# Optimization experiments

Hardware: AMD Instinct MI355X
Metric: run time of the kernel (lower is better)

The kernel has to match this reference:

```python
import jax, jax.numpy as jnp
import numpy as np
from jax import lax

B, N, S, K = 8, 8192, 2048, 32
CPTS = 64
RADIUS = 0.25
MLP = [64, 64, 128]
EPS = 1e-5


def fps(xyz, npoint):
    # furthest point sampling, starts at index 0 (pointnet2 convention)
    Bn, Nn, _ = xyz.shape

    def step(carry, _):
        mind, last = carry  # mind [B,N], last [B]
        lastp = jnp.take_along_axis(xyz, last[:, None, None], axis=1)  # [B,1,3]
        d = jnp.sum((xyz - lastp) ** 2, axis=-1)  # [B,N]
        mind = jnp.minimum(mind, d)
        nxt = jnp.argmax(mind, axis=-1).astype(jnp.int32)
        return (mind, nxt), last

    init = (jnp.full((Bn, Nn), 1e10, xyz.dtype), jnp.zeros((Bn,), jnp.int32))
    _, idxs = lax.scan(step, init, None, length=npoint)  # [npoint,B]
    return jnp.transpose(idxs)  # [B,npoint]


def ball_query(radius, nsample, xyz, new_xyz):
    # returns first `nsample` indices within radius of each centroid,
    # padding with the first valid index (pointnet2 semantics)
    Nn = xyz.shape[1]
    qq = jnp.sum(new_xyz ** 2, -1)[:, :, None]          # [B,S,1]
    pp = jnp.sum(xyz ** 2, -1)[:, None, :]              # [B,1,N]
    d2 = qq + pp - 2.0 * jnp.einsum('bsc,bnc->bsn', new_xyz, xyz)  # [B,S,N]
    key = jnp.where(d2 <= radius * radius,
                    jnp.arange(Nn, dtype=jnp.int32), jnp.int32(Nn))
    srt = jnp.sort(key, axis=-1)[..., :nsample]          # first valid indices
    return jnp.where(srt < Nn, srt, srt[..., :1])        # pad with first


def _gather(feats, idx):
    # feats [B,N,C], idx [B,S,K] -> [B,S,K,C]
    return jax.vmap(lambda p, i: p[i])(feats, idx)


def setup_inputs() -> dict:
    key = jax.random.key(0)
    ks = jax.random.split(key, 2 + len(MLP))
    xyz = jax.random.normal(ks[0], (B, N, 3), jnp.float32)
    points = jax.random.normal(ks[1], (B, N, CPTS), jnp.float32)
    out = {"xyz": xyz, "points": points}
    cin = 3 + CPTS
    for i, m in enumerate(MLP):
        out[f"w{i}"] = jax.random.normal(ks[2 + i], (m, cin), jnp.float32) * 0.05
        out[f"b{i}"] = jnp.zeros((m,), jnp.float32)
        out[f"g{i}"] = jnp.ones((m,), jnp.float32)
        out[f"be{i}"] = jnp.zeros((m,), jnp.float32)
        cin = m
    return out


def reference(xyz, points, w0, b0, g0, be0, w1, b1, g1, be1, w2, b2, g2, be2):
    fps_idx = fps(xyz, S)                                    # [B,S]
    new_xyz = jnp.take_along_axis(xyz, fps_idx[..., None], axis=1)  # [B,S,3]
    idx = ball_query(RADIUS, K, xyz, new_xyz)                # [B,S,K]

    grouped_xyz = _gather(xyz, idx) - new_xyz[:, :, None, :]  # [B,S,K,3]
    grouped_pts = _gather(points, idx)                        # [B,S,K,CPTS]
    feat = jnp.concatenate([grouped_xyz, grouped_pts], -1)    # [B,S,K,C]

    for (w, b, g, be) in ((w0, b0, g0, be0), (w1, b1, g1, be1), (w2, b2, g2, be2)):
        x = jnp.einsum('bskc,oc->bsko', feat, w) + b           # 1x1 conv
        mean = jnp.mean(x, axis=(0, 1, 2))                     # BN train-mode
        var = jnp.var(x, axis=(0, 1, 2))
        feat = jax.nn.relu((x - mean) * jax.lax.rsqrt(var + EPS) * g + be)

    pooled = jnp.max(feat, axis=2)                             # [B,S,Cout]
    return new_xyz, pooled
```

## Files before the change

kernel.cpp:

```cpp
#include <hip/hip_runtime.h>

#define NPTS 8192
#define NB 8
#define NS 2048
#define NK 32
#define C0 67
#define NTOT (NB*NS*NK)
#define NCONS 248

typedef __attribute__((ext_vector_type(2))) float f32x2;

template <int CTRL, int ROWM>
__device__ __forceinline__ float dpp_fmax_step(float x) {
  int yi = __builtin_amdgcn_update_dpp(__float_as_int(x), __float_as_int(x),
                                       CTRL, ROWM, 0xf, false);
  return fmaxf(x, __int_as_float(yi));
}
template <int CTRL, int ROWM>
__device__ __forceinline__ unsigned dpp_umin_step(unsigned x) {
  unsigned y = (unsigned)__builtin_amdgcn_update_dpp((int)x, (int)x,
                                                     CTRL, ROWM, 0xf, false);
  return (y < x) ? y : x;
}
__device__ __forceinline__ float wave_max_f32(float v) {
  v = dpp_fmax_step<0x111, 0xf>(v);
  v = dpp_fmax_step<0x112, 0xf>(v);
  v = dpp_fmax_step<0x114, 0xf>(v);
  v = dpp_fmax_step<0x118, 0xf>(v);
  v = dpp_fmax_step<0x142, 0xa>(v);
  v = dpp_fmax_step<0x143, 0xc>(v);
  return v;
}
__device__ __forceinline__ unsigned wave_min_u32(unsigned v) {
  v = dpp_umin_step<0x111, 0xf>(v);
  v = dpp_umin_step<0x112, 0xf>(v);
  v = dpp_umin_step<0x114, 0xf>(v);
  v = dpp_umin_step<0x118, 0xf>(v);
  v = dpp_umin_step<0x142, 0xa>(v);
  v = dpp_umin_step<0x143, 0xc>(v);
  return v;
}

union SMemA {
  struct {
    float sx[NPTS], sy[NPTS], sz[NPTS];
    float snx[NS], sny[NS], snz[NS];
    uint2 slotVN[2][4];
  } fps;
  struct {
    float w0t[C0*64];
    float feat[C0*32];
    int   bq[4][32];
    int   bqc[4];
    int   s_idx[32];
    float s_c[3];
  } con;
};

__global__ __launch_bounds__(256, 1) void k_stage1A(
    const float* __restrict__ xyz, const float* __restrict__ pts,
    const float* __restrict__ w0, const float* __restrict__ g0,
    const float* __restrict__ be0,
    float* __restrict__ newxyz, float* __restrict__ pp,
    float* __restrict__ x0, float* __restrict__ part,
    float* __restrict__ statsF, unsigned* __restrict__ sync) {
  __shared__ __align__(16) SMemA sm;
  __shared__ int s_last;
  const int tid = threadIdx.x;
  unsigned* prog = sync;
  unsigned* ctr0 = sync + 8;

  if (blockIdx.x < NB) {
    const int b = blockIdx.x;
    const int wv = tid >> 6, lane = tid & 63;
    const float* Xb = xyz + (size_t)b * NPTS * 3;
    f32x2 px2[16], py2[16], pz2[16], mind2[16];
#pragma unroll
    for (int i = 0; i < 16; i++) {
      int n0 = ((2*i) << 8) | tid;
      int n1 = ((2*i+1) << 8) | tid;
      float ax = Xb[n0*3+0], ay = Xb[n0*3+1], az = Xb[n0*3+2];
      float bx2 = Xb[n1*3+0], by2 = Xb[n1*3+1], bz2 = Xb[n1*3+2];
      px2[i].x = ax;  px2[i].y = bx2;
      py2[i].x = ay;  py2[i].y = by2;
      pz2[i].x = az;  pz2[i].y = bz2;
      sm.fps.sx[n0]=ax;  sm.fps.sy[n0]=ay;  sm.fps.sz[n0]=az;
      sm.fps.sx[n1]=bx2; sm.fps.sy[n1]=by2; sm.fps.sz[n1]=bz2;
      pp[b*NPTS + n0] = __fadd_rn(__fadd_rn(__fmul_rn(ax,ax), __fmul_rn(ay,ay)), __fmul_rn(az,az));
      pp[b*NPTS + n1] = __fadd_rn(__fadd_rn(__fmul_rn(bx2,bx2), __fmul_rn(by2,by2)), __fmul_rn(bz2,bz2));
      mind2[i].x = 1e10f; mind2[i].y = 1e10f;
    }
    __syncthreads();
    float lx = sm.fps.sx[0], ly = sm.fps.sy[0], lz = sm.fps.sz[0];
    if (tid == 0) { sm.fps.snx[0]=lx; sm.fps.sny[0]=ly; sm.fps.snz[0]=lz; }
    for (int s = 1; s < NS; s++) {
#pragma clang fp contract(off)
      f32x2 lxx = {lx, lx}, lyy = {ly, ly}, lzz = {lz, lz};
      f32x2 m16[16];
#pragma unroll
      for (int i = 0; i < 16; i++) {
        f32x2 dx = px2[i] - lxx;
        f32x2 dy = py2[i] - lyy;
        f32x2 dz = pz2[i] - lzz;
        f32x2 d  = (dx*dx + dy*dy) + dz*dz;
        f32x2 m;
        m.x = fminf(mind2[i].x, d.x);
        m.y = fminf(mind2[i].y, d.y);
        mind2[i] = m;
        m16[i] = m;
      }
#pragma unroll
      for (int st = 8; st >= 1; st >>= 1)
#pragma unroll
        for (int i = 0; i < st; i++) {
          m16[i].x = fmaxf(m16[i].x, m16[i+st].x);
          m16[i].y = fmaxf(m16[i].y, m16[i+st].y);
        }
      float v = fmaxf(m16[0].x, m16[0].y);
      float vr = wave_max_f32(v);
      float wmax = __int_as_float(__builtin_amdgcn_readlane(__float_as_int(vr), 63));
      unsigned kt[16];
#pragma unroll
      for (int i = 0; i < 16; i++) {
        unsigned c = (mind2[i].y == v) ? (unsigned)(2*i+1) : 63u;
        kt[i] = (mind2[i].x == v) ? (unsigned)(2*i) : c;
      }
#pragma unroll
      for (int st = 8; st >= 1; st >>= 1)
#pragma unroll
        for (int i = 0; i < st; i++)
          kt[i] = (kt[i] < kt[i+st]) ? kt[i] : kt[i+st];
      unsigned ncand = (v == wmax) ? ((kt[0] << 8) | (unsigned)tid) : 0xffffffffu;
      unsigned nr = wave_min_u32(ncand);
      int buf = s & 1;
      if (lane == 63) sm.fps.slotVN[buf][wv] = make_uint2(__float_as_uint(vr), nr);
      __syncthreads();
      uint4 s01 = *(const uint4*)&sm.fps.slotVN[buf][0];
      uint4 s23 = *(const uint4*)&sm.fps.slotVN[buf][2];
      unsigned bx = s01.x, by = s01.y;
      if (s01.z > bx || (s01.z == bx && s01.w < by)) { bx = s01.z; by = s01.w; }
      if (s23.x > bx || (s23.x == bx && s23.y < by)) { bx = s23.x; by = s23.y; }
      if (s23.z > bx || (s23.z == bx && s23.w < by)) { bx = s23.z; by = s23.w; }
      int n = (int)by;
      lx = sm.fps.sx[n]; ly = sm.fps.sy[n]; lz = sm.fps.sz[n];
      if (tid == 0) { sm.fps.snx[s]=lx; sm.fps.sny[s]=ly; sm.fps.snz[s]=lz; }
      if ((s & 63) == 63) {
        __syncthreads();
        int cs = s - 63;
        if (tid < 192) {
          int e = cs + tid / 3, comp = tid - (tid / 3) * 3;
          float vvv = (comp == 0) ? sm.fps.snx[e] : ((comp == 1) ? sm.fps.sny[e] : sm.fps.snz[e]);
          newxyz[((size_t)b*NS + cs)*3 + tid] = vvv;
        }
        __syncthreads();
        if (tid == 0) {
          __threadfence();
          __hip_atomic_store(&prog[b], (unsigned)(s + 1), __ATOMIC_RELEASE, __HIP_MEMORY_SCOPE_AGENT);
        }
      }
    }
  } else {
    const int cb = blockIdx.x - NB;
    const int wv = tid >> 6, lane = tid & 63;
    float* w0t = sm.con.w0t;
    float* feat = sm.con.feat;
    for (int t = tid; t < C0*64; t += 256) { int j = t >> 6, c = t & 63; w0t[t] = w0[c*C0 + j]; }
    int rt = tid & 7, ct = tid >> 3;
    float s0[2] = {0,0}, q0[2] = {0,0};
    for (int it = 0; it <= 66; it++) {
      int e = cb + NCONS * it;
      if (e >= NB*NS) break;
      int s = e >> 3, b = e & 7;
      size_t row = (size_t)b * NS + s;
      if (tid == 0) {
        while ((int)__hip_atomic_load(&prog[b], __ATOMIC_ACQUIRE, __HIP_MEMORY_SCOPE_AGENT) <= s)
          __builtin_amdgcn_s_sleep(32);
        __threadfence();
      }
      __syncthreads();
      const float* c3 = newxyz + row * 3;
      float cx = c3[0], cy = c3[1], cz = c3[2];
      float qq = __fadd_rn(__fadd_rn(__fmul_rn(cx,cx), __fmul_rn(cy,cy)), __fmul_rn(cz,cz));
      const float* Xb = xyz + (size_t)b * NPTS * 3;
      const float* Pb = pp + b * NPTS;
      int cnt = 0;
      int base = wv << 11;
      for (int j0 = base; j0 < base + 2048; j0 += 64) {
        int n = j0 + lane;
        float x = Xb[n*3+0], y = Xb[n*3+1], z = Xb[n*3+2];
        float dot = __fadd_rn(__fadd_rn(__fmul_rn(cx,x), __fmul_rn(cy,y)), __fmul_rn(cz,z));
        float d2 = __fsub_rn(__fadd_rn(qq, Pb[n]), __fmul_rn(2.0f, dot));
        bool in = (d2 <= 0.0625f);
        unsigned long long bal = __ballot(in);
        if (in) {
          int pos = cnt + (int)__popcll(bal & ((1ull << lane) - 1ull));
          if (pos < NK) sm.con.bq[wv][pos] = n;
        }
        cnt += (int)__popcll(bal);
        if (cnt >= NK) break;
      }
      if (lane == 0) sm.con.bqc[wv] = (cnt < NK) ? cnt : NK;
      __syncthreads();
      if (tid < NK) {
        int l0 = sm.con.bqc[0], l1 = sm.con.bqc[1], l2 = sm.con.bqc[2], l3 = sm.con.bqc[3];
        int t1 = l0 + l1, t2 = t1 + l2, t3 = t2 + l3;
        int j = tid, v;
        if (j < l0)      v = sm.con.bq[0][j];
        else if (j < t1) v = sm.con.bq[1][j - l0];
        else if (j < t2) v = sm.con.bq[2][j - t1];
        else if (j < t3) v = sm.con.bq[3][j - t2];
        else {
          v = (l0 > 0) ? sm.con.bq[0][0] : (l1 > 0) ? sm.con.bq[1][0]
            : (l2 > 0) ? sm.con.bq[2][0] : (l3 > 0) ? sm.con.bq[3][0] : 0;
        }
        sm.con.s_idx[j] = v;
      }
      if (tid >= 32 && tid < 35) sm.con.s_c[tid - 32] = c3[tid - 32];
      __syncthreads();
      if (tid < 32) {
        const float* p = &xyz[((size_t)b*NPTS + sm.con.s_idx[tid])*3];
        feat[0*32+tid] = p[0] - sm.con.s_c[0];
        feat[1*32+tid] = p[1] - sm.con.s_c[1];
        feat[2*32+tid] = p[2] - sm.con.s_c[2];
      }
      {
        int r_ = tid & 31, cq_ = tid >> 5;
        const float* pr = &pts[((size_t)b*NPTS + sm.con.s_idx[r_])*64 + cq_*8];
        float4 A_ = *(const float4*)pr;
        float4 B_ = *(const float4*)(pr + 4);
        feat[(3+cq_*8+0)*32 + r_] = A_.x;
        feat[(3+cq_*8+1)*32 + r_] = A_.y;
        feat[(3+cq_*8+2)*32 + r_] = A_.z;
        feat[(3+cq_*8+3)*32 + r_] = A_.w;
        feat[(3+cq_*8+4)*32 + r_] = B_.x;
        feat[(3+cq_*8+5)*32 + r_] = B_.y;
        feat[(3+cq_*8+6)*32 + r_] = B_.z;
        feat[(3+cq_*8+7)*32 + r_] = B_.w;
      }
      __syncthreads();
      float acc[4][2] = {};
      for (int j = 0; j < C0; j++) {
        float4 av = *(const float4*)&feat[j*32 + rt*4];
        float2 wvv = *(const float2*)&w0t[j*64 + ct*2];
        float aa[4] = {av.x, av.y, av.z, av.w};
#pragma unroll
        for (int r = 0; r < 4; r++) {
          acc[r][0] = fmaf(aa[r], wvv.x, acc[r][0]);
          acc[r][1] = fmaf(aa[r], wvv.y, acc[r][1]);
        }
      }
      float* dst = x0 + row * 2048;
#pragma unroll
      for (int r = 0; r < 4; r++)
#pragma unroll
        for (int u = 0; u < 2; u++) {
          float x = acc[r][u];
          dst[(rt*4+r)*64 + ct*2+u] = x;
          s0[u] += x; q0[u] = fmaf(x, x, q0[u]);
        }
      __syncthreads();
    }
#pragma unroll
    for (int off = 1; off < 8; off <<= 1) {
#pragma unroll
      for (int u = 0; u < 2; u++) { s0[u] += __shfl_xor(s0[u], off, 64); q0[u] += __shfl_xor(q0[u], off, 64); }
    }
    if (rt == 0) {
#pragma unroll
      for (int u = 0; u < 2; u++) {
        size_t o = ((size_t)cb * 128 + ct*2 + u) * 2;
        part[o] = s0[u]; part[o+1] = q0[u];
      }
    }
    __threadfence();
    if (tid == 0) {
      unsigned old = __hip_atomic_fetch_add(ctr0, 1u, __ATOMIC_ACQ_REL, __HIP_MEMORY_SCOPE_AGENT);
      s_last = (old == NCONS - 1);
    }
    __syncthreads();
    if (s_last) {
      __threadfence();
      if (tid < 64) {
        float s = 0.f, q = 0.f;
        for (int k = 0; k < NCONS; k++) {
          s += part[((size_t)k * 128 + tid) * 2];
          q += part[((size_t)k * 128 + tid) * 2 + 1];
        }
        const float inv = 1.0f / (float)NTOT;
        float mean = s * inv;
        float var = q * inv - mean * mean;
        float a = g0[tid] / sqrtf(var + 1e-5f);
        float bb = be0[tid] - mean * a;
        statsF[tid*2] = a; statsF[tid*2 + 1] = bb;
      }
    }
  }
}

__global__ __launch_bounds__(256) void k_l1x(
    float* __restrict__ x0, const float* __restrict__ w1,
    const float* __restrict__ g1, const float* __restrict__ be1,
    float* __restrict__ statsF, float* __restrict__ part,
    unsigned* __restrict__ sync) {
  __shared__ __align__(16) float w1t[64*64];
  __shared__ __align__(16) float x0n[64*32];
  __shared__ float sF[128];
  __shared__ int s_last;
  unsigned* ctr1 = sync + 9;
  int tid = threadIdx.x;
  for (int t = tid; t < 64*64; t += 256) { int j = t >> 6, c = t & 63; w1t[t] = w1[c*64 + j]; }
  if (tid < 64) { sF[tid] = statsF[tid*2]; sF[64+tid] = statsF[tid*2+1]; }
  int rt = tid & 7, ct = tid >> 3;
  float s1[2] = {0,0}, q1[2] = {0,0};
  for (int g = 0; g < 32; g++) {
    size_t gid = (size_t)blockIdx.x * 32 + g;
    __syncthreads();
    float* src = x0 + gid * 2048;
#pragma unroll
    for (int i = 0; i < 2; i++) {
      int local = tid*8 + i*4;
      float4 v = *(const float4*)(src + local);
      int row = local >> 6, col = local & 63;
      x0n[(col+0)*32+row] = fmaxf(0.f, fmaf(v.x, sF[col+0], sF[64+col+0]));
      x0n[(col+1)*32+row] = fmaxf(0.f, fmaf(v.y, sF[col+1], sF[64+col+1]));
      x0n[(col+2)*32+row] = fmaxf(0.f, fmaf(v.z, sF[col+2], sF[64+col+2]));
      x0n[(col+3)*32+row] = fmaxf(0.f, fmaf(v.w, sF[col+3], sF[64+col+3]));
    }
    __syncthreads();
    float acc[4][2] = {};
    for (int j = 0; j < 64; j++) {
      float4 av = *(const float4*)&x0n[j*32 + rt*4];
      float2 wv = *(const float2*)&w1t[j*64 + ct*2];
      float aa[4] = {av.x, av.y, av.z, av.w};
#pragma unroll
      for (int r = 0; r < 4; r++) {
        acc[r][0] = fmaf(aa[r], wv.x, acc[r][0]);
        acc[r][1] = fmaf(aa[r], wv.y, acc[r][1]);
      }
    }
#pragma unroll
    for (int r = 0; r < 4; r++)
#pragma unroll
      for (int u = 0; u < 2; u++) {
        float x = acc[r][u];
        src[(rt*4+r)*64 + ct*2+u] = x;
        s1[u] += x; q1[u] = fmaf(x, x, q1[u]);
      }
  }
#pragma unroll
  for (int off = 1; off < 8; off <<= 1) {
#pragma unroll
    for (int u = 0; u < 2; u++) { s1[u] += __shfl_xor(s1[u], off, 64); q1[u] += __shfl_xor(q1[u], off, 64); }
  }
  if (rt == 0) {
#pragma unroll
    for (int u = 0; u < 2; u++) {
      size_t o = ((size_t)blockIdx.x * 128 + ct*2 + u) * 2;
      part[o] = s1[u]; part[o+1] = q1[u];
    }
  }
  __threadfence();
  if (tid == 0) {
    unsigned old = __hip_atomic_fetch_add(ctr1, 1u, __ATOMIC_ACQ_REL, __HIP_MEMORY_SCOPE_AGENT);
    s_last = (old == 511);
  }
  __syncthreads();
  if (s_last) {
    __threadfence();
    if (tid < 64) {
      float s = 0.f, q = 0.f;
      for (int k = 0; k < 512; k++) {
        s += part[((size_t)k * 128 + tid) * 2];
        q += part[((size_t)k * 128 + tid) * 2 + 1];
      }
      const float inv = 1.0f / (float)NTOT;
      float mean = s * inv;
      float var = q * inv - mean * mean;
      float a = g1[tid] / sqrtf(var + 1e-5f);
      float bb = be1[tid] - mean * a;
      statsF[(128 + tid)*2] = a; statsF[(128 + tid)*2 + 1] = bb;
    }
  }
}

__global__ __launch_bounds__(256) void k_l2x(
    const float* __restrict__ x1, const float* __restrict__ w2,
    const float* __restrict__ g2, const float* __restrict__ be2,
    float* __restrict__ statsF, float* __restrict__ part,
    float* __restrict__ maxb, float* __restrict__ minb,
    unsigned* __restrict__ sync) {
  __shared__ __align__(16) float w2t[64*128];
  __shared__ __align__(16) float x1n[64*32];
  __shared__ float sF[128];
  __shared__ int s_last;
  unsigned* ctr2 = sync + 10;
  int tid = threadIdx.x;
  for (int t = tid; t < 64*128; t += 256) { int j = t >> 7, c = t & 127; w2t[t] = w2[c*64 + j]; }
  if (tid < 64) { sF[tid] = statsF[(128+tid)*2]; sF[64+tid] = statsF[(128+tid)*2+1]; }
  int rt = tid & 7, ct = tid >> 3;
  float s2[4] = {0,0,0,0}, q2[4] = {0,0,0,0};
  for (int g = 0; g < 64; g++) {
    size_t gid = (size_t)blockIdx.x * 64 + g;
    __syncthreads();
    const float* src = x1 + gid * 2048;
#pragma unroll
    for (int i = 0; i < 2; i++) {
      int local = tid*8 + i*4;
      float4 v = *(const float4*)(src + local);
      int row = local >> 6, col = local & 63;
      x1n[(col+0)*32+row] = fmaxf(0.f, fmaf(v.x, sF[col+0], sF[64+col+0]));
      x1n[(col+1)*32+row] = fmaxf(0.f, fmaf(v.y, sF[col+1], sF[64+col+1]));
      x1n[(col+2)*32+row] = fmaxf(0.f, fmaf(v.z, sF[col+2], sF[64+col+2]));
      x1n[(col+3)*32+row] = fmaxf(0.f, fmaf(v.w, sF[col+3], sF[64+col+3]));
    }
    __syncthreads();
    float acc[4][4] = {};
    for (int j = 0; j < 64; j++) {
      float4 av = *(const float4*)&x1n[j*32 + rt*4];
      float4 wvv = *(const float4*)&w2t[j*128 + ct*4];
      float aa[4] = {av.x, av.y, av.z, av.w};
      float ww[4] = {wvv.x, wvv.y, wvv.z, wvv.w};
#pragma unroll
      for (int r = 0; r < 4; r++)
#pragma unroll
        for (int u = 0; u < 4; u++) acc[r][u] = fmaf(aa[r], ww[u], acc[r][u]);
    }
    float mx[4], mn[4];
#pragma unroll
    for (int u = 0; u < 4; u++) {
      float x0v = acc[0][u], x1v = acc[1][u], x2v = acc[2][u], x3v = acc[3][u];
      s2[u] += ((x0v + x1v) + (x2v + x3v));
      q2[u] = fmaf(x0v, x0v, q2[u]); q2[u] = fmaf(x1v, x1v, q2[u]);
      q2[u] = fmaf(x2v, x2v, q2[u]); q2[u] = fmaf(x3v, x3v, q2[u]);
      mx[u] = fmaxf(fmaxf(x0v, x1v), fmaxf(x2v, x3v));
      mn[u] = fminf(fminf(x0v, x1v), fminf(x2v, x3v));
    }
#pragma unroll
    for (int off = 1; off < 8; off <<= 1) {
#pragma unroll
      for (int u = 0; u < 4; u++) {
        mx[u] = fmaxf(mx[u], __shfl_xor(mx[u], off, 64));
        mn[u] = fminf(mn[u], __shfl_xor(mn[u], off, 64));
      }
    }
    if (rt == 0) {
#pragma unroll
      for (int u = 0; u < 4; u++) {
        maxb[gid*128 + ct*4 + u] = mx[u];
        minb[gid*128 + ct*4 + u] = mn[u];
      }
    }
  }
#pragma unroll
  for (int off = 1; off < 8; off <<= 1) {
#pragma unroll
    for (int u = 0; u < 4; u++) { s2[u] += __shfl_xor(s2[u], off, 64); q2[u] += __shfl_xor(q2[u], off, 64); }
  }
  if (rt == 0) {
#pragma unroll
    for (int u = 0; u < 4; u++) {
      size_t o = ((size_t)blockIdx.x * 128 + ct*4 + u) * 2;
      part[o] = s2[u]; part[o+1] = q2[u];
    }
  }
  __threadfence();
  if (tid == 0) {
    unsigned old = __hip_atomic_fetch_add(ctr2, 1u, __ATOMIC_ACQ_REL, __HIP_MEMORY_SCOPE_AGENT);
    s_last = (old == 255);
  }
  __syncthreads();
  if (s_last) {
    __threadfence();
    if (tid < 128) {
      float s = 0.f, q = 0.f;
      for (int k = 0; k < 256; k++) {
        s += part[((size_t)k * 128 + tid) * 2];
        q += part[((size_t)k * 128 + tid) * 2 + 1];
      }
      const float inv = 1.0f / (float)NTOT;
      float mean = s * inv;
      float var = q * inv - mean * mean;
      float a = g2[tid] / sqrtf(var + 1e-5f);
      float bb = be2[tid] - mean * a;
      statsF[(256 + tid)*2] = a; statsF[(256 + tid)*2 + 1] = bb;
    }
  }
}

__global__ __launch_bounds__(256) void k_pool(const float* __restrict__ maxb,
                                              const float* __restrict__ minb,
                                              const float* __restrict__ statsF,
                                              float* __restrict__ outp) {
  int t = blockIdx.x * 256 + threadIdx.x;
  int c = t & 127;
  float a  = statsF[(2*128 + c)*2];
  float bb = statsF[(2*128 + c)*2 + 1];
  float X = (a >= 0.f) ? maxb[t] : minb[t];
  outp[t] = fmaxf(0.f, fmaf(a, X, bb));
}

extern "C" void kernel_launch(void* const* d_in, const int* in_sizes, int n_in,
                              void* d_out, int out_size, void* d_ws, size_t ws_size,
                              hipStream_t stream) {
  (void)in_sizes; (void)n_in; (void)out_size; (void)ws_size;
  const float* xyz = (const float*)d_in[0];
  const float* pts = (const float*)d_in[1];
  const float* w0  = (const float*)d_in[2];
  const float* g0  = (const float*)d_in[4];
  const float* be0 = (const float*)d_in[5];
  const float* w1  = (const float*)d_in[6];
  const float* g1  = (const float*)d_in[8];
  const float* be1 = (const float*)d_in[9];
  const float* w2  = (const float*)d_in[10];
  const float* g2  = (const float*)d_in[12];
  const float* be2 = (const float*)d_in[13];

  float* out = (float*)d_out;
  float* newxyz = out;
  float* pooled = out + (size_t)NB*NS*3;

  float* ws = (float*)d_ws;
  float* pp     = ws;
  float* x0     = ws + 65536;
  float* part   = x0 + 33554432;
  float* statsF = part + 131072;
  float* maxb   = statsF + 768;
  float* minb   = maxb + 2097152;
  unsigned* sync = (unsigned*)(minb + 2097152);

  hipMemsetAsync(sync, 0, 64, stream);
  k_stage1A<<<256, 256, 0, stream>>>(xyz, pts, w0, g0, be0,
                                     newxyz, pp, x0, part, statsF, sync);
  k_l1x<<<512, 256, 0, stream>>>(x0, w1, g1, be1, statsF, part, sync);
  k_l2x<<<256, 256, 0, stream>>>(x0, w2, g2, be2, statsF, part,
                                 maxb, minb, sync);
  k_pool<<<8192, 256, 0, stream>>>(maxb, minb, statsF, pooled);
}
```

Before: 2.662 ms.

## Double block size: FPS over 8 waves, consumers process two centroids per block

Widens the fused stage-1 kernel to 512 threads. FPS blocks now spread the points over 8 waves with half the register state per thread and merge eight wave winners per step. Consumer blocks split into two 256-thread halves that each handle a separate centroid with their own shared buffers, which doubles the number of partial-stat slots. The aim is to shorten the serial FPS step latency and raise consumer throughput, at the cost of a wider per-step block barrier in FPS and shared barriers that couple the two consumer halves.

```diff
diff --git a/kernel.cpp b/kernel.cpp
--- a/kernel.cpp
+++ b/kernel.cpp
@@ -7,6 +7,8 @@
 #define C0 67
 #define NTOT (NB*NS*NK)
 #define NCONS 248
+#define NHALF 496
+#define NITER 34
 
 typedef __attribute__((ext_vector_type(2))) float f32x2;
 
@@ -45,19 +47,19 @@
   struct {
     float sx[NPTS], sy[NPTS], sz[NPTS];
     float snx[NS], sny[NS], snz[NS];
-    uint2 slotVN[2][4];
+    uint2 slotVN[2][8];
   } fps;
   struct {
     float w0t[C0*64];
-    float feat[C0*32];
-    int   bq[4][32];
-    int   bqc[4];
-    int   s_idx[32];
-    float s_c[3];
+    float feat[2][C0*32];
+    int   bq[2][4][32];
+    int   bqc[2][4];
+    int   s_idx[2][32];
+    float s_c[2][3];
   } con;
 };
 
-__global__ __launch_bounds__(256, 1) void k_stage1A(
+__global__ __launch_bounds__(512, 2) void k_stage1A(
     const float* __restrict__ xyz, const float* __restrict__ pts,
     const float* __restrict__ w0, const float* __restrict__ g0,
     const float* __restrict__ be0,
@@ -74,11 +76,11 @@
     const int b = blockIdx.x;
     const int wv = tid >> 6, lane = tid & 63;
     const float* Xb = xyz + (size_t)b * NPTS * 3;
-    f32x2 px2[16], py2[16], pz2[16], mind2[16];
-#pragma unroll
-    for (int i = 0; i < 16; i++) {
-      int n0 = ((2*i) << 8) | tid;
-      int n1 = ((2*i+1) << 8) | tid;
+    f32x2 px2[8], py2[8], pz2[8], mind2[8];
+#pragma unroll
+    for (int i = 0; i < 8; i++) {
+      int n0 = ((2*i) << 9) | tid;
+      int n1 = ((2*i+1) << 9) | tid;
       float ax = Xb[n0*3+0], ay = Xb[n0*3+1], az = Xb[n0*3+2];
       float bx2 = Xb[n1*3+0], by2 = Xb[n1*3+1], bz2 = Xb[n1*3+2];
       px2[i].x = ax;  px2[i].y = bx2;
@@ -96,9 +98,9 @@
     for (int s = 1; s < NS; s++) {
 #pragma clang fp contract(off)
       f32x2 lxx = {lx, lx}, lyy = {ly, ly}, lzz = {lz, lz};
-      f32x2 m16[16];
-#pragma unroll
-      for (int i = 0; i < 16; i++) {
+      f32x2 m16[8];
+#pragma unroll
+      for (int i = 0; i < 8; i++) {
         f32x2 dx = px2[i] - lxx;
         f32x2 dy = py2[i] - lyy;
         f32x2 dz = pz2[i] - lzz;
@@ -110,7 +112,7 @@
         m16[i] = m;
       }
 #pragma unroll
-      for (int st = 8; st >= 1; st >>= 1)
+      for (int st = 4; st >= 1; st >>= 1)
 #pragma unroll
         for (int i = 0; i < st; i++) {
           m16[i].x = fmaxf(m16[i].x, m16[i+st].x);
@@ -119,29 +121,38 @@
       float v = fmaxf(m16[0].x, m16[0].y);
       float vr = wave_max_f32(v);
       float wmax = __int_as_float(__builtin_amdgcn_readlane(__float_as_int(vr), 63));
-      unsigned kt[16];
-#pragma unroll
-      for (int i = 0; i < 16; i++) {
+      unsigned kt[8];
+#pragma unroll
+      for (int i = 0; i < 8; i++) {
         unsigned c = (mind2[i].y == v) ? (unsigned)(2*i+1) : 63u;
         kt[i] = (mind2[i].x == v) ? (unsigned)(2*i) : c;
       }
 #pragma unroll
-      for (int st = 8; st >= 1; st >>= 1)
+      for (int st = 4; st >= 1; st >>= 1)
 #pragma unroll
         for (int i = 0; i < st; i++)
           kt[i] = (kt[i] < kt[i+st]) ? kt[i] : kt[i+st];
-      unsigned ncand = (v == wmax) ? ((kt[0] << 8) | (unsigned)tid) : 0xffffffffu;
+      unsigned ncand = (v == wmax) ? ((kt[0] << 9) | (unsigned)tid) : 0xffffffffu;
       unsigned nr = wave_min_u32(ncand);
       int buf = s & 1;
       if (lane == 63) sm.fps.slotVN[buf][wv] = make_uint2(__float_as_uint(vr), nr);
       __syncthreads();
-      uint4 s01 = *(const uint4*)&sm.fps.slotVN[buf][0];
-      uint4 s23 = *(const uint4*)&sm.fps.slotVN[buf][2];
-      unsigned bx = s01.x, by = s01.y;
-      if (s01.z > bx || (s01.z == bx && s01.w < by)) { bx = s01.z; by = s01.w; }
-      if (s23.x > bx || (s23.x == bx && s23.y < by)) { bx = s23.x; by = s23.y; }
-      if (s23.z > bx || (s23.z == bx && s23.w < by)) { bx = s23.z; by = s23.w; }
-      int n = (int)by;
+      uint4 q0 = *(const uint4*)&sm.fps.slotVN[buf][0];
+      uint4 q1 = *(const uint4*)&sm.fps.slotVN[buf][2];
+      uint4 q2 = *(const uint4*)&sm.fps.slotVN[buf][4];
+      uint4 q3 = *(const uint4*)&sm.fps.slotVN[buf][6];
+      unsigned v0 = q0.x, n0_ = q0.y;
+      if (q0.z > v0 || (q0.z == v0 && q0.w < n0_)) { v0 = q0.z; n0_ = q0.w; }
+      unsigned v1 = q1.x, n1_ = q1.y;
+      if (q1.z > v1 || (q1.z == v1 && q1.w < n1_)) { v1 = q1.z; n1_ = q1.w; }
+      unsigned v2 = q2.x, n2_ = q2.y;
+      if (q2.z > v2 || (q2.z == v2 && q2.w < n2_)) { v2 = q2.z; n2_ = q2.w; }
+      unsigned v3 = q3.x, n3_ = q3.y;
+      if (q3.z > v3 || (q3.z == v3 && q3.w < n3_)) { v3 = q3.z; n3_ = q3.w; }
+      if (v1 > v0 || (v1 == v0 && n1_ < n0_)) { v0 = v1; n0_ = n1_; }
+      if (v3 > v2 || (v3 == v2 && n3_ < n2_)) { v2 = v3; n2_ = n3_; }
+      if (v2 > v0 || (v2 == v0 && n2_ < n0_)) { v0 = v2; n0_ = n2_; }
+      int n = (int)n0_;
       lx = sm.fps.sx[n]; ly = sm.fps.sy[n]; lz = sm.fps.sz[n];
       if (tid == 0) { sm.fps.snx[s]=lx; sm.fps.sny[s]=ly; sm.fps.snz[s]=lz; }
       if ((s & 63) == 63) {
@@ -161,115 +172,126 @@
     }
   } else {
     const int cb = blockIdx.x - NB;
-    const int wv = tid >> 6, lane = tid & 63;
+    const int h = tid >> 8;
+    const int t = tid & 255;
+    const int wv = (tid >> 6) & 3, lane = tid & 63;
     float* w0t = sm.con.w0t;
-    float* feat = sm.con.feat;
-    for (int t = tid; t < C0*64; t += 256) { int j = t >> 6, c = t & 63; w0t[t] = w0[c*C0 + j]; }
-    int rt = tid & 7, ct = tid >> 3;
-    float s0[2] = {0,0}, q0[2] = {0,0};
-    for (int it = 0; it <= 66; it++) {
-      int e = cb + NCONS * it;
-      if (e >= NB*NS) break;
+    float* feat = sm.con.feat[h];
+    for (int i = tid; i < C0*64; i += 512) { int j = i >> 6, c = i & 63; w0t[i] = w0[c*C0 + j]; }
+    int rt = t & 7, ct = t >> 3;
+    float s0[2] = {0,0}, q0s[2] = {0,0};
+    for (int it = 0; it < NITER; it++) {
+      int e = (cb << 1) + h + NHALF * it;
+      bool active = (e < NB*NS);
       int s = e >> 3, b = e & 7;
       size_t row = (size_t)b * NS + s;
-      if (tid == 0) {
+      if (active && t == 0) {
         while ((int)__hip_atomic_load(&prog[b], __ATOMIC_ACQUIRE, __HIP_MEMORY_SCOPE_AGENT) <= s)
           __builtin_amdgcn_s_sleep(32);
         __threadfence();
       }
       __syncthreads();
       const float* c3 = newxyz + row * 3;
-      float cx = c3[0], cy = c3[1], cz = c3[2];
-      float qq = __fadd_rn(__fadd_rn(__fmul_rn(cx,cx), __fmul_rn(cy,cy)), __fmul_rn(cz,cz));
-      const float* Xb = xyz + (size_t)b * NPTS * 3;
-      const float* Pb = pp + b * NPTS;
-      int cnt = 0;
-      int base = wv << 11;
-      for (int j0 = base; j0 < base + 2048; j0 += 64) {
-        int n = j0 + lane;
-        float x = Xb[n*3+0], y = Xb[n*3+1], z = Xb[n*3+2];
-        float dot = __fadd_rn(__fadd_rn(__fmul_rn(cx,x), __fmul_rn(cy,y)), __fmul_rn(cz,z));
-        float d2 = __fsub_rn(__fadd_rn(qq, Pb[n]), __fmul_rn(2.0f, dot));
-        bool in = (d2 <= 0.0625f);
-        unsigned long long bal = __ballot(in);
-        if (in) {
-          int pos = cnt + (int)__popcll(bal & ((1ull << lane) - 1ull));
-          if (pos < NK) sm.con.bq[wv][pos] = n;
-        }
-        cnt += (int)__popcll(bal);
-        if (cnt >= NK) break;
-      }
-      if (lane == 0) sm.con.bqc[wv] = (cnt < NK) ? cnt : NK;
+      float cx = 0.f, cy = 0.f, cz = 0.f, qq = 0.f;
+      if (active) {
+        cx = c3[0]; cy = c3[1]; cz = c3[2];
+        qq = __fadd_rn(__fadd_rn(__fmul_rn(cx,cx), __fmul_rn(cy,cy)), __fmul_rn(cz,cz));
+        const float* Xb = xyz + (size_t)b * NPTS * 3;
+        const float* Pb = pp + b * NPTS;
+        int cnt = 0;
+        int base = wv << 11;
+        for (int j0 = base; j0 < base + 2048; j0 += 64) {
+          int n = j0 + lane;
+          float x = Xb[n*3+0], y = Xb[n*3+1], z = Xb[n*3+2];
+          float dot = __fadd_rn(__fadd_rn(__fmul_rn(cx,x), __fmul_rn(cy,y)), __fmul_rn(cz,z));
+          float d2 = __fsub_rn(__fadd_rn(qq, Pb[n]), __fmul_rn(2.0f, dot));
+          bool in = (d2 <= 0.0625f);
+          unsigned long long bal = __ballot(in);
+          if (in) {
+            int pos = cnt + (int)__popcll(bal & ((1ull << lane) - 1ull));
+            if (pos < NK) sm.con.bq[h][wv][pos] = n;
+          }
+          cnt += (int)__popcll(bal);
+          if (cnt >= NK) break;
+        }
+        if (lane == 0) sm.con.bqc[h][wv] = (cnt < NK) ? cnt : NK;
+      }
       __syncthreads();
-      if (tid < NK) {
-        int l0 = sm.con.bqc[0], l1 = sm.con.bqc[1], l2 = sm.con.bqc[2], l3 = sm.con.bqc[3];
-        int t1 = l0 + l1, t2 = t1 + l2, t3 = t2 + l3;
-        int j = tid, v;
-        if (j < l0)      v = sm.con.bq[0][j];
-        else if (j < t1) v = sm.con.bq[1][j - l0];
-        else if (j < t2) v = sm.con.bq[2][j - t1];
-        else if (j < t3) v = sm.con.bq[3][j - t2];
-        else {
-          v = (l0 > 0) ? sm.con.bq[0][0] : (l1 > 0) ? sm.con.bq[1][0]
-            : (l2 > 0) ? sm.con.bq[2][0] : (l3 > 0) ? sm.con.bq[3][0] : 0;
-        }
-        sm.con.s_idx[j] = v;
-      }
-      if (tid >= 32 && tid < 35) sm.con.s_c[tid - 32] = c3[tid - 32];
+      if (active) {
+        if (t < NK) {
+          int l0 = sm.con.bqc[h][0], l1 = sm.con.bqc[h][1], l2 = sm.con.bqc[h][2], l3 = sm.con.bqc[h][3];
+          int t1 = l0 + l1, t2 = t1 + l2, t3 = t2 + l3;
+          int j = t, v;
+          if (j < l0)      v = sm.con.bq[h][0][j];
+          else if (j < t1) v = sm.con.bq[h][1][j - l0];
+          else if (j < t2) v = sm.con.bq[h][2][j - t1];
+          else if (j < t3) v = sm.con.bq[h][3][j - t2];
+          else {
+            v = (l0 > 0) ? sm.con.bq[h][0][0] : (l1 > 0) ? sm.con.bq[h][1][0]
+              : (l2 > 0) ? sm.con.bq[h][2][0] : (l3 > 0) ? sm.con.bq[h][3][0] : 0;
+          }
+          sm.con.s_idx[h][j] = v;
+        }
+        if (t >= 32 && t < 35) sm.con.s_c[h][t - 32] = c3[t - 32];
+      }
       __syncthreads();
-      if (tid < 32) {
-        const float* p = &xyz[((size_t)b*NPTS + sm.con.s_idx[tid])*3];
-        feat[0*32+tid] = p[0] - sm.con.s_c[0];
-        feat[1*32+tid] = p[1] - sm.con.s_c[1];
-        feat[2*32+tid] = p[2] - sm.con.s_c[2];
-      }
-      {
-        int r_ = tid & 31, cq_ = tid >> 5;
-        const float* pr = &pts[((size_t)b*NPTS + sm.con.s_idx[r_])*64 + cq_*8];
-        float4 A_ = *(const float4*)pr;
-        float4 B_ = *(const float4*)(pr + 4);
-        feat[(3+cq_*8+0)*32 + r_] = A_.x;
-        feat[(3+cq_*8+1)*32 + r_] = A_.y;
-        feat[(3+cq_*8+2)*32 + r_] = A_.z;
-        feat[(3+cq_*8+3)*32 + r_] = A_.w;
-        feat[(3+cq_*8+4)*32 + r_] = B_.x;
-        feat[(3+cq_*8+5)*32 + r_] = B_.y;
-        feat[(3+cq_*8+6)*32 + r_] = B_.z;
-        feat[(3+cq_*8+7)*32 + r_] = B_.w;
+      if (active) {
+        if (t < 32) {
+          const float* p = &xyz[((size_t)b*NPTS + sm.con.s_idx[h][t])*3];
+          feat[0*32+t] = p[0] - sm.con.s_c[h][0];
+          feat[1*32+t] = p[1] - sm.con.s_c[h][1];
+          feat[2*32+t] = p[2] - sm.con.s_c[h][2];
+        }
+        {
+          int r_ = t & 31, cq_ = t >> 5;
+          const float* pr = &pts[((size_t)b*NPTS + sm.con.s_idx[h][r_])*64 + cq_*8];
+          float4 A_ = *(const float4*)pr;
+          float4 B_ = *(const float4*)(pr + 4);
+          feat[(3+cq_*8+0)*32 + r_] = A_.x;
+          feat[(3+cq_*8+1)*32 + r_] = A_.y;
+          feat[(3+cq_*8+2)*32 + r_] = A_.z;
+          feat[(3+cq_*8+3)*32 + r_] = A_.w;
+          feat[(3+cq_*8+4)*32 + r_] = B_.x;
+          feat[(3+cq_*8+5)*32 + r_] = B_.y;
+          feat[(3+cq_*8+6)*32 + r_] = B_.z;
+          feat[(3+cq_*8+7)*32 + r_] = B_.w;
+        }
       }
       __syncthreads();
-      float acc[4][2] = {};
-      for (int j = 0; j < C0; j++) {
-        float4 av = *(const float4*)&feat[j*32 + rt*4];
-        float2 wvv = *(const float2*)&w0t[j*64 + ct*2];
-        float aa[4] = {av.x, av.y, av.z, av.w};
-#pragma unroll
-        for (int r = 0; r < 4; r++) {
-          acc[r][0] = fmaf(aa[r], wvv.x, acc[r][0]);
-          acc[r][1] = fmaf(aa[r], wvv.y, acc[r][1]);
-        }
-      }
-      float* dst = x0 + row * 2048;
-#pragma unroll
-      for (int r = 0; r < 4; r++)
-#pragma unroll
-        for (int u = 0; u < 2; u++) {
-          float x = acc[r][u];
-          dst[(rt*4+r)*64 + ct*2+u] = x;
-          s0[u] += x; q0[u] = fmaf(x, x, q0[u]);
-        }
+      if (active) {
+        float acc[4][2] = {};
+        for (int j = 0; j < C0; j++) {
+          float4 av = *(const float4*)&feat[j*32 + rt*4];
+          float2 wvv = *(const float2*)&w0t[j*64 + ct*2];
+          float aa[4] = {av.x, av.y, av.z, av.w};
+#pragma unroll
+          for (int r = 0; r < 4; r++) {
+            acc[r][0] = fmaf(aa[r], wvv.x, acc[r][0]);
+            acc[r][1] = fmaf(aa[r], wvv.y, acc[r][1]);
+          }
+        }
+        float* dst = x0 + row * 2048;
+#pragma unroll
+        for (int r = 0; r < 4; r++)
+#pragma unroll
+          for (int u = 0; u < 2; u++) {
+            float x = acc[r][u];
+            dst[(rt*4+r)*64 + ct*2+u] = x;
+            s0[u] += x; q0s[u] = fmaf(x, x, q0s[u]);
+          }
+      }
       __syncthreads();
     }
 #pragma unroll
     for (int off = 1; off < 8; off <<= 1) {
 #pragma unroll
-      for (int u = 0; u < 2; u++) { s0[u] += __shfl_xor(s0[u], off, 64); q0[u] += __shfl_xor(q0[u], off, 64); }
+      for (int u = 0; u < 2; u++) { s0[u] += __shfl_xor(s0[u], off, 64); q0s[u] += __shfl_xor(q0s[u], off, 64); }
     }
     if (rt == 0) {
 #pragma unroll
       for (int u = 0; u < 2; u++) {
-        size_t o = ((size_t)cb * 128 + ct*2 + u) * 2;
-        part[o] = s0[u]; part[o+1] = q0[u];
+        size_t o = ((size_t)((cb << 1) + h) * 128 + ct*2 + u) * 2;
+        part[o] = s0[u]; part[o+1] = q0s[u];
       }
     }
     __threadfence();
@@ -282,7 +304,7 @@
       __threadfence();
       if (tid < 64) {
         float s = 0.f, q = 0.f;
-        for (int k = 0; k < NCONS; k++) {
+        for (int k = 0; k < NHALF; k++) {
           s += part[((size_t)k * 128 + tid) * 2];
           q += part[((size_t)k * 128 + tid) * 2 + 1];
         }
@@ -529,7 +551,7 @@
   unsigned* sync = (unsigned*)(minb + 2097152);
 
   hipMemsetAsync(sync, 0, 64, stream);
-  k_stage1A<<<256, 256, 0, stream>>>(xyz, pts, w0, g0, be0,
+  k_stage1A<<<256, 512, 0, stream>>>(xyz, pts, w0, g0, be0,
                                      newxyz, pp, x0, part, statsF, sync);
   k_l1x<<<512, 256, 0, stream>>>(x0, w1, g1, be1, statsF, part, sync);
   k_l2x<<<256, 256, 0, stream>>>(x0, w2, g2, be2, statsF, part,
```

Measured after the change: 2.949 ms. 10.8% more time.
